# Optimization experiments

Hardware: AMD Instinct MI355X
Metric: run time of the kernel (lower is better)

Reference implementation:

```python
import jax, jax.numpy as jnp
import numpy as np

B, NPG, NFEAT, NHID, NCLASS = 32, 256, 128, 64, 6
N = B * NPG
E_PER = NPG * 16
C = 1.0
SQC = 1.0  # sqrt(c)
MIN_NORM = 1e-15
PROJ_EPS = 4e-3
LAMB = 1.0


def _norm(x):
    return jnp.clip(jnp.linalg.norm(x, axis=-1, keepdims=True), MIN_NORM)


def artanh(x):
    x = jnp.clip(x, -1.0 + 1e-7, 1.0 - 1e-7)
    return 0.5 * (jnp.log1p(x) - jnp.log1p(-x))


def proj(x):
    # clip points to stay inside the Poincare ball
    n = _norm(x)
    maxn = (1.0 - PROJ_EPS) / SQC
    return jnp.where(n > maxn, x / n * maxn, x)


def expmap0(u):
    un = _norm(u)
    return jnp.tanh(SQC * un) * u / (SQC * un)


def logmap0(p):
    pn = _norm(p)
    return artanh(SQC * pn) * p / (SQC * pn)


def mobius_matvec(W, x):
    xn = _norm(x)
    mx = x @ W.T
    mxn = _norm(mx)
    return jnp.tanh(mxn / xn * artanh(SQC * xn)) * mx / (mxn * SQC)


def mobius_add(x, y):
    x2 = jnp.sum(x * x, -1, keepdims=True)
    y2 = jnp.sum(y * y, -1, keepdims=True)
    xy = jnp.sum(x * y, -1, keepdims=True)
    num = (1.0 + 2.0 * C * xy + C * y2) * x + (1.0 - C * x2) * y
    den = 1.0 + 2.0 * C * xy + C * C * x2 * y2
    return num / jnp.clip(den, MIN_NORM)


def hgc_layer(xh, adj, W, b):
    # HypLinear (mobius matvec + hyperbolic bias)
    h = proj(mobius_matvec(W, xh))
    hb = proj(expmap0(b.reshape(1, -1)))
    h = proj(mobius_add(h, hb))
    # HypAgg: aggregate in tangent space at origin
    h = proj(expmap0(adj @ logmap0(h)))
    # HypAct: relu in tangent space
    return proj(expmap0(jax.nn.relu(logmap0(h))))


def hgpsl_pool(x, adj, att, nb, npg):
    deg = adj.sum(-1)
    dis = jnp.where(deg > 0, deg ** -0.5, 0.0)
    prop = dis[:, None] * (adj @ (dis[:, None] * x))
    score = jnp.abs(x - prop).sum(-1)  # [N]
    k = npg // 2
    vals, idx = jax.lax.top_k(score.reshape(nb, npg), k)  # per-graph top-k
    gidx = (idx + (jnp.arange(nb) * npg)[:, None]).reshape(-1)  # global ids
    xn = x[gidx] * jnp.tanh(vals).reshape(-1, 1)
    adj_ind = adj[gidx][:, gidx]
    # structure learning: single-head additive attention, masked per graph
    d = xn.shape[-1]
    e = jax.nn.leaky_relu((xn @ att[:d])[:, None] + (xn @ att[d:])[None, :], 0.2)
    gid = jnp.repeat(jnp.arange(nb), k)
    mask = gid[:, None] == gid[None, :]
    new_adj = jnp.where(mask, jax.nn.relu(e) + LAMB * adj_ind, 0.0)
    return xn, new_adj


def readout(x, nb, k):
    xr = x.reshape(nb, k, -1)
    return jnp.concatenate([xr.max(axis=1), xr.mean(axis=1)], axis=-1)


def to_hyp(t):
    return proj(expmap0(t))  # proj_tan0 is identity on the Poincare ball


def forward(x, edge_index, W1, b1, W2, b2, W3, b3, att1, att2,
            lw1, lb1, lw2, lb2, lw3, lb3):
    row, col = edge_index[0], edge_index[1]
    w = (x[row].sum(-1) + x[col].sum(-1)) * 0.5
    adj1 = jnp.zeros((N, N), x.dtype).at[row, col].set(w)

    t = logmap0(hgc_layer(to_hyp(x), adj1, W1, b1))
    t, adj2 = hgpsl_pool(t, adj1, att1, B, NPG)
    k1 = NPG // 2
    x1 = readout(t, B, k1)

    t = logmap0(hgc_layer(to_hyp(t), adj2, W2, b2))
    t, adj3 = hgpsl_pool(t, adj2, att2, B, k1)
    k2 = k1 // 2
    x2 = readout(t, B, k2)

    t = logmap0(hgc_layer(to_hyp(t), adj3, W3, b3))
    x3 = readout(t, B, k2)

    r = jax.nn.relu(x1) + jax.nn.relu(x2) + jax.nn.relu(x3)
    r = jax.nn.relu(r @ lw1.T + lb1)
    r = jax.nn.relu(r @ lw2.T + lb2)
    return jax.nn.log_softmax(r @ lw3.T + lb3, axis=-1)


def setup_inputs() -> dict:
    key = jax.random.key(0)
    ks = jax.random.split(key, 16)
    s = 0.1
    x = jax.random.normal(ks[0], (N, NFEAT), jnp.float32)
    off = jnp.repeat(jnp.arange(B, dtype=jnp.int32) * NPG, E_PER)
    row = jax.random.randint(ks[1], (B * E_PER,), 0, NPG, jnp.int32) + off
    col = jax.random.randint(ks[2], (B * E_PER,), 0, NPG, jnp.int32) + off
    edge_index = jnp.stack([row, col])
    return {
        "x": x,
        "edge_index": edge_index,
        "W1": jax.random.normal(ks[3], (NHID, NFEAT), jnp.float32) * s,
        "b1": jax.random.normal(ks[4], (NHID,), jnp.float32) * s,
        "W2": jax.random.normal(ks[5], (NHID, NHID), jnp.float32) * s,
        "b2": jax.random.normal(ks[6], (NHID,), jnp.float32) * s,
        "W3": jax.random.normal(ks[7], (NHID, NHID), jnp.float32) * s,
        "b3": jax.random.normal(ks[8], (NHID,), jnp.float32) * s,
        "att1": jax.random.normal(ks[9], (2 * NHID,), jnp.float32) * s,
        "att2": jax.random.normal(ks[10], (2 * NHID,), jnp.float32) * s,
        "lw1": jax.random.normal(ks[11], (NHID, 2 * NHID), jnp.float32) * s,
        "lb1": jnp.zeros((NHID,), jnp.float32),
        "lw2": jax.random.normal(ks[12], (NHID // 2, NHID), jnp.float32) * s,
        "lb2": jnp.zeros((NHID // 2,), jnp.float32),
        "lw3": jax.random.normal(ks[13], (NCLASS, NHID // 2), jnp.float32) * s,
        "lb3": jnp.zeros((NCLASS,), jnp.float32),
    }


def reference(x, edge_index, W1, b1, W2, b2, W3, b3, att1, att2,
              lw1, lb1, lw2, lb2, lw3, lb3):
    return forward(x, edge_index, W1, b1, W2, b2, W3, b3, att1, att2,
                   lw1, lb1, lw2, lb2, lw3, lb3)
```

## Files before the change

kernel.cpp:

```cpp
#include <hip/hip_runtime.h>
#include <math.h>

#define MAXN 0.996f

typedef float f32x4 __attribute__((ext_vector_type(4)));

__device__ __forceinline__ float wredsum(float v) {
#pragma unroll
  for (int o = 32; o > 0; o >>= 1) v += __shfl_xor(v, o);
  return v;
}

__device__ __forceinline__ float artanh_f(float x) {
  x = fminf(fmaxf(x, -1.0f + 1e-7f), 1.0f - 1e-7f);
  return 0.5f * (log1pf(x) - log1pf(-x));
}

__device__ __forceinline__ float cload(const float* p) {
  return __hip_atomic_load(p, __ATOMIC_RELAXED, __HIP_MEMORY_SCOPE_AGENT);
}
__device__ __forceinline__ int cloadi(const int* p) {
  return __hip_atomic_load(p, __ATOMIC_RELAXED, __HIP_MEMORY_SCOPE_AGENT);
}
__device__ __forceinline__ void cstore(float* p, float v) {
  __hip_atomic_store(p, v, __ATOMIC_RELAXED, __HIP_MEMORY_SCOPE_AGENT);
}
__device__ __forceinline__ void cstorei(int* p, int v) {
  __hip_atomic_store(p, v, __ATOMIC_RELAXED, __HIP_MEMORY_SCOPE_AGENT);
}
__device__ __forceinline__ void cstore128(float* p, float a, float b, float c,
                                          float d) {
  f32x4 v;
  v.x = a; v.y = b; v.z = c; v.w = d;
  asm volatile("global_store_dwordx4 %0, %1, off sc0 sc1" ::"v"(p), "v"(v)
               : "memory");
}
__device__ __forceinline__ void quadStore(float* base, int j, float v) {
  float v1 = __shfl_xor(v, 1);
  float v2 = __shfl_xor(v, 2);
  float v3 = __shfl_xor(v, 3);
  if ((j & 3) == 0) cstore128(base + j, v, v1, v2, v3);
}
template <int N>
__device__ __forceinline__ void stage64(float* dst, const float* src, int tid) {
  const unsigned long long* s = (const unsigned long long*)src;
  unsigned long long* d = (unsigned long long*)dst;
  unsigned long long v[N];
#pragma unroll
  for (int k = 0; k < N; ++k)
    v[k] = __hip_atomic_load(s + tid + k * 1024, __ATOMIC_RELAXED,
                             __HIP_MEMORY_SCOPE_AGENT);
#pragma unroll
  for (int k = 0; k < N; ++k) d[tid + k * 1024] = v[k];
}

__device__ __forceinline__ float chainB(float acc) {
  float n0 = sqrtf(wredsum(acc * acc));
  float u0 = fmaxf(n0, 1e-15f);
  float e1 = tanhf(u0) / u0;
  float c1 = fmaxf(e1 * n0, 1e-15f);
  float v = acc * e1;
  if (c1 > MAXN) { v *= MAXN / c1; c1 = MAXN; }
  v *= artanh_f(c1) / c1;
  v = fmaxf(v, 0.f);
  float n2 = sqrtf(wredsum(v * v));
  float u2 = fmaxf(n2, 1e-15f);
  float e2 = tanhf(u2) / u2;
  float c2 = fmaxf(e2 * n2, 1e-15f);
  v *= e2;
  if (c2 > MAXN) { v *= MAXN / c2; c2 = MAXN; }
  v *= artanh_f(c2) / c2;
  return v;
}

__device__ __forceinline__ void hbCalc(int j, const float* __restrict__ b,
                                       float& hbj, float& y2) {
  float bj = b[j];
  float nb = sqrtf(wredsum(bj * bj));
  float ub = fmaxf(nb, 1e-15f);
  float eb = tanhf(ub) / ub;
  float cb = fmaxf(eb * nb, 1e-15f);
  hbj = bj * eb * ((cb > MAXN) ? MAXN / cb : 1.0f);
  y2 = wredsum(hbj * hbj);
}

template <int IND>
__device__ __forceinline__ void doArow(int j, const float* xs, const float* wT,
                                       float hbj, float y2,
                                       float* __restrict__ uout) {
  float a2 = xs[j] * xs[j];
  if (IND == 128) { float x1v = xs[64 + j]; a2 += x1v * x1v; }
  float nx = sqrtf(wredsum(a2));
  float un = fmaxf(nx, 1e-15f);
  float s1 = tanhf(un) / un;
  float nv = s1 * nx;
  float nn = fmaxf(nv, 1e-15f);
  float s2 = (nn > MAXN) ? MAXN / nn : 1.0f;
  float alpha = s1 * s2;
  float xn = fmaxf(fminf(nn, MAXN), 1e-15f);

  float y = 0.f;
  for (int t = 0; t < IND; ++t) y = fmaf(xs[t], wT[t * 65 + j], y);
  float mxj = alpha * y;
  float mxn = fmaxf(sqrtf(wredsum(mxj * mxj)), 1e-15f);
  float hj = (tanhf(mxn / xn * artanh_f(xn)) / mxn) * mxj;

  float hn = fmaxf(sqrtf(wredsum(hj * hj)), 1e-15f);
  if (hn > MAXN) hj *= MAXN / hn;

  float x2 = wredsum(hj * hj);
  float xy = wredsum(hj * hbj);
  float num = (1.f + 2.f * xy + y2) * hj + (1.f - x2) * hbj;
  float den = fmaxf(1.f + 2.f * xy + x2 * y2, 1e-15f);
  float aj = num / den;

  float an = fmaxf(sqrtf(wredsum(aj * aj)), 1e-15f);
  float pn = an;
  if (an > MAXN) { aj *= MAXN / an; pn = MAXN; }
  quadStore(uout, j, (artanh_f(pn) / pn) * aj);
}

template <int NP, int TR, bool WANTDIS>
__device__ __forceinline__ void doBgrpL(int j, int r0, int r0l,
                                        const float* adjS, const float* uS,
                                        float* __restrict__ tg,
                                        float* __restrict__ disg) {
  float acc[TR], dsum[TR];
#pragma unroll
  for (int r = 0; r < TR; ++r) { acc[r] = 0.f; dsum[r] = 0.f; }
  for (int c0 = 0; c0 < NP; c0 += 4) {
    float uv0 = uS[(c0 + 0) * 64 + j];
    float uv1 = uS[(c0 + 1) * 64 + j];
    float uv2 = uS[(c0 + 2) * 64 + j];
    float uv3 = uS[(c0 + 3) * 64 + j];
#pragma unroll
    for (int r = 0; r < TR; ++r) {
      const float4 a4 = *(const float4*)(adjS + (r0l + r) * NP + c0);
      acc[r] = fmaf(a4.x, uv0, acc[r]);
      acc[r] = fmaf(a4.y, uv1, acc[r]);
      acc[r] = fmaf(a4.z, uv2, acc[r]);
      acc[r] = fmaf(a4.w, uv3, acc[r]);
      if (WANTDIS) {
        dsum[r] += a4.x; dsum[r] += a4.y; dsum[r] += a4.z; dsum[r] += a4.w;
      }
    }
  }
#pragma unroll
  for (int r = 0; r < TR; ++r) {
    float v = chainB(acc[r]);
    quadStore(tg + (size_t)(r0 + r) * 64, j, v);
    if (WANTDIS && j == 0)
      cstore(disg + r0 + r, (dsum[r] > 0.f) ? (1.0f / sqrtf(dsum[r])) : 0.f);
  }
}

template <int NP, int TR>
__device__ __forceinline__ void doCgrpL(int j, int r0, int r0l,
                                        const float* adjS, const float* tS,
                                        const float* disS,
                                        float* __restrict__ scoreg) {
  float acc[TR];
#pragma unroll
  for (int r = 0; r < TR; ++r) acc[r] = 0.f;
  for (int c0 = 0; c0 < NP; c0 += 4) {
    float uv0 = disS[c0 + 0] * tS[(c0 + 0) * 64 + j];
    float uv1 = disS[c0 + 1] * tS[(c0 + 1) * 64 + j];
    float uv2 = disS[c0 + 2] * tS[(c0 + 2) * 64 + j];
    float uv3 = disS[c0 + 3] * tS[(c0 + 3) * 64 + j];
#pragma unroll
    for (int r = 0; r < TR; ++r) {
      const float4 a4 = *(const float4*)(adjS + (r0l + r) * NP + c0);
      acc[r] = fmaf(a4.x, uv0, acc[r]);
      acc[r] = fmaf(a4.y, uv1, acc[r]);
      acc[r] = fmaf(a4.z, uv2, acc[r]);
      acc[r] = fmaf(a4.w, uv3, acc[r]);
    }
  }
#pragma unroll
  for (int r = 0; r < TR; ++r) {
    float d = fabsf(tS[(r0 + r) * 64 + j] - disS[r0 + r] * acc[r]);
    d = wredsum(d);
    if (j == 0) cstore(scoreg + r0 + r, d);
  }
}

template <int NP>
__device__ __forceinline__ void doDEa(int j, int i, const float* scS,
                                      const float* tS,
                                      const float* __restrict__ att,
                                      float* __restrict__ xng,
                                      float* __restrict__ s1g,
                                      float* __restrict__ s2g,
                                      int* __restrict__ selg) {
  constexpr int K = NP / 2;
  float si = scS[i];
  float cnt = 0.f;
#pragma unroll
  for (int kk = 0; kk < NP / 64; ++kk) {
    int c = j + kk * 64;
    float v = scS[c];
    cnt += ((v > si) || (v == si && c < i)) ? 1.f : 0.f;
  }
  int rank = (int)wredsum(cnt);
  if (rank < K) {
    float tv = tanhf(si);
    float v = tS[i * 64 + j] * tv;
    quadStore(xng + (size_t)rank * 64, j, v);
    float a = wredsum(v * att[j]);
    float b2 = wredsum(v * att[64 + j]);
    if (j == 0) {
      cstore(s1g + rank, a);
      cstore(s2g + rank, b2);
      cstorei(selg + rank, i);
    }
  }
}

template <int K>
__device__ __forceinline__ void doReadoutL(int j, const float* __restrict__ xng,
                                           float* xrl) {
  float mx = -1e30f, sm = 0.f;
#pragma unroll
  for (int r = 0; r < K; ++r) {
    float v = cload(xng + (size_t)r * 64 + j);
    mx = fmaxf(mx, v);
    sm += v;
  }
  xrl[j] = mx;
  xrl[64 + j] = sm * (1.0f / K);
}

__device__ __forceinline__ void cluster_bar(int* bar, int target, int tid) {
  __syncthreads();
  if (tid == 0) {
    __hip_atomic_fetch_add(bar, 1, __ATOMIC_RELAXED, __HIP_MEMORY_SCOPE_AGENT);
    while (__hip_atomic_load(bar, __ATOMIC_RELAXED, __HIP_MEMORY_SCOPE_AGENT) <
           target * 8)
      __builtin_amdgcn_s_sleep(2);
  }
  __syncthreads();
}

struct KP {
  const float* x; const int* ei; int nE;
  const float *W1, *b1, *W2, *b2, *W3, *b3, *att1, *att2;
  const float *lw1, *lb1, *lw2, *lb2, *lw3, *lb3;
  float *adj2, *adj3, *ubuf, *t1, *t2, *t3, *srow, *dis, *score;
  float *xn1, *xn2, *s1b, *s2b;
  int *sel, *bar;
  float* out;
};

__global__ void __launch_bounds__(1024, 4) k_fwd(KP P) {
  const int tid = threadIdx.x;
  const int wib = tid >> 6;
  const int j = tid & 63;
  const int g = blockIdx.x >> 3;
  const int lb = blockIdx.x & 7;
  const int wc = lb * 16 + wib;

  __shared__ float wT[128 * 65];
  __shared__ float xsAll[16 * 128];
  __shared__ float stage[16384];
  __shared__ float adjS[8192];
  __shared__ float scS[256];
  __shared__ float s1S[128];
  __shared__ float s2S[128];
  __shared__ int selS[128];
  __shared__ float x12S[256];
  float* xs = xsAll + wib * 128;

  int* bar = P.bar + g * 64;
  float* adj2g = P.adj2 + (size_t)g * 16384;
  float* adj3g = P.adj3 + (size_t)g * 4096;
  const float* xg = P.x + (size_t)g * 32768;
  float* srowg = P.srow + g * 256;
  float* ubufg = P.ubuf + (size_t)g * 16384;
  float* t1g = P.t1 + (size_t)g * 16384;
  float* t2g = P.t2 + (size_t)g * 8192;
  float* t3g = P.t3 + (size_t)g * 4096;
  float* disg = P.dis + g * 256;
  float* scoreg = P.score + g * 256;
  float* xn1g = P.xn1 + (size_t)g * 8192;
  float* xn2g = P.xn2 + (size_t)g * 4096;
  float* s1g = P.s1b + g * 128;
  float* s2g = P.s2b + g * 128;
  int* selg = P.sel + g * 128;

  {
    for (int idx = tid; idx < 8192; idx += 1024)
      wT[(idx & 127) * 65 + (idx >> 7)] = P.W1[idx];
    for (int k = tid; k < 8192; k += 1024) adjS[k] = 0.f;
    float hbj, y2;
    hbCalc(j, P.b1, hbj, y2);
    for (int rr = 0; rr < 2; ++rr) {
      const int row = lb * 32 + wib * 2 + rr;
      xs[j] = xg[(size_t)row * 128 + j];
      xs[64 + j] = xg[(size_t)row * 128 + 64 + j];
      float a = xs[j] + xs[64 + j];
      a = wredsum(a);
      if (j == 0) cstore(srowg + row, a);
      doArow<128>(j, xs, wT, hbj, y2, ubufg + (size_t)row * 64);
    }
  }
  cluster_bar(bar, 1, tid);

  {
    if (tid < 256) scS[tid] = cload(srowg + tid);
    stage64<8>(stage, ubufg, tid);
    __syncthreads();
    const int epg = P.nE >> 5;
    for (int e = g * epg + tid; e < (g + 1) * epg; e += 1024) {
      int r = P.ei[e] & 255;
      if ((r >> 5) == lb) {
        int c = P.ei[P.nE + e] & 255;
        adjS[(r & 31) * 256 + c] = 0.5f * (scS[r] + scS[c]);
      }
    }
    __syncthreads();
    doBgrpL<256, 2, true>(j, lb * 32 + wib * 2, wib * 2, adjS, stage, t1g,
                          disg);
    for (int idx = tid; idx < 4096; idx += 1024)
      wT[(idx & 63) * 65 + (idx >> 6)] = P.W2[idx];
  }
  cluster_bar(bar, 2, tid);

  {
    if (tid < 256) scS[tid] = cload(disg + tid);
    stage64<8>(stage, t1g, tid);
    __syncthreads();
    doCgrpL<256, 2>(j, lb * 32 + wib * 2, wib * 2, adjS, stage, scS, scoreg);
  }
  cluster_bar(bar, 3, tid);

  {
    if (tid < 256) scS[tid] = cload(scoreg + tid);
    __syncthreads();
    for (int row = wc; row < 256; row += 128)
      doDEa<256>(j, row, scS, stage, P.att1, xn1g, s1g, s2g, selg);
  }
  cluster_bar(bar, 4, tid);

  {
    if (tid < 128) {
      s1S[tid] = cload(s1g + tid);
      s2S[tid] = cload(s2g + tid);
      selS[tid] = cloadi(selg + tid);
    }
    __syncthreads();
    for (int q = tid; q < 4096; q += 1024) {
      int ii = q >> 5, jj0 = (q & 31) * 4;
      int sii = selS[ii];
      if ((sii >> 5) == lb) {
        const float* arow = adjS + (sii & 31) * 256;
        float s1v = s1S[ii];
        float v0 = fmaxf(s1v + s2S[jj0 + 0], 0.f) + arow[selS[jj0 + 0]];
        float v1 = fmaxf(s1v + s2S[jj0 + 1], 0.f) + arow[selS[jj0 + 1]];
        float v2 = fmaxf(s1v + s2S[jj0 + 2], 0.f) + arow[selS[jj0 + 2]];
        float v3 = fmaxf(s1v + s2S[jj0 + 3], 0.f) + arow[selS[jj0 + 3]];
        cstore128(adj2g + ii * 128 + jj0, v0, v1, v2, v3);
      }
    }
    if (wc == 0) doReadoutL<128>(j, xn1g, x12S);
    float hbj, y2;
    hbCalc(j, P.b2, hbj, y2);
    {
      int row = wc;
      xs[j] = cload(xn1g + (size_t)row * 64 + j);
      doArow<64>(j, xs, wT, hbj, y2, ubufg + (size_t)row * 64);
    }
  }
  cluster_bar(bar, 5, tid);

  {
    stage64<1>(adjS, adj2g + lb * 2048, tid);
    stage64<4>(stage, ubufg, tid);
    __syncthreads();
    doBgrpL<128, 1, true>(j, wc, wib, adjS, stage, t2g, disg);
    for (int idx = tid; idx < 4096; idx += 1024)
      wT[(idx & 63) * 65 + (idx >> 6)] = P.W3[idx];
  }
  cluster_bar(bar, 6, tid);

  {
    if (tid < 128) scS[tid] = cload(disg + tid);
    stage64<4>(stage, t2g, tid);
    __syncthreads();
    doCgrpL<128, 1>(j, wc, wib, adjS, stage, scS, scoreg);
  }
  cluster_bar(bar, 7, tid);

  {
    if (tid < 128) scS[tid] = cload(scoreg + tid);
    __syncthreads();
    doDEa<128>(j, wc, scS, stage, P.att2, xn2g, s1g, s2g, selg);
  }
  cluster_bar(bar, 8, tid);

  {
    if (tid < 64) {
      s1S[tid] = cload(s1g + tid);
      s2S[tid] = cload(s2g + tid);
      selS[tid] = cloadi(selg + tid);
    }
    __syncthreads();
    {
      int ii = tid >> 4, jj0 = (tid & 15) * 4;
      int sii = selS[ii];
      if ((sii >> 4) == lb) {
        const float* arow = adjS + (sii & 15) * 128;
        float s1v = s1S[ii];
        float v0 = fmaxf(s1v + s2S[jj0 + 0], 0.f) + arow[selS[jj0 + 0]];
        float v1 = fmaxf(s1v + s2S[jj0 + 1], 0.f) + arow[selS[jj0 + 1]];
        float v2 = fmaxf(s1v + s2S[jj0 + 2], 0.f) + arow[selS[jj0 + 2]];
        float v3 = fmaxf(s1v + s2S[jj0 + 3], 0.f) + arow[selS[jj0 + 3]];
        cstore128(adj3g + ii * 64 + jj0, v0, v1, v2, v3);
      }
    }
    if (wc == 0) doReadoutL<64>(j, xn2g, x12S + 128);
    float hbj, y2;
    hbCalc(j, P.b3, hbj, y2);
    if (wc < 64) {
      int row = wc;
      xs[j] = cload(xn2g + (size_t)row * 64 + j);
      doArow<64>(j, xs, wT, hbj, y2, ubufg + (size_t)row * 64);
    }
  }
  cluster_bar(bar, 9, tid);

  if (lb < 4) {
    if (tid < 512) {
      unsigned long long v = __hip_atomic_load(
          (const unsigned long long*)(adj3g + lb * 1024) + tid,
          __ATOMIC_RELAXED, __HIP_MEMORY_SCOPE_AGENT);
      ((unsigned long long*)adjS)[tid] = v;
    }
    stage64<2>(stage, ubufg, tid);
    __syncthreads();
    doBgrpL<64, 1, false>(j, wc, wib, adjS, stage, t3g, nullptr);
  }
  cluster_bar(bar, 10, tid);

  if (wc == 0) {
    float mx = -1e30f, sm = 0.f;
#pragma unroll
    for (int r = 0; r < 64; ++r) {
      float v = cload(t3g + (size_t)r * 64 + j);
      mx = fmaxf(mx, v);
      sm += v;
    }
    float* S = xsAll;
    S[j] = fmaxf(x12S[j], 0.f) + fmaxf(x12S[128 + j], 0.f) + fmaxf(mx, 0.f);
    S[64 + j] = fmaxf(x12S[64 + j], 0.f) + fmaxf(x12S[192 + j], 0.f) +
                fmaxf(sm * (1.0f / 64.0f), 0.f);
    float acc = P.lb1[j];
    for (int t = 0; t < 128; ++t) acc += S[t] * P.lw1[(size_t)j * 128 + t];
    S[128 + j] = fmaxf(acc, 0.f);
    if (j < 32) {
      float a = P.lb2[j];
      for (int t = 0; t < 64; ++t) a += S[128 + t] * P.lw2[(size_t)j * 64 + t];
      S[192 + j] = fmaxf(a, 0.f);
    }
    if (j < 6) {
      float a = P.lb3[j];
      for (int t = 0; t < 32; ++t) a += S[192 + t] * P.lw3[(size_t)j * 32 + t];
      S[224 + j] = a;
    }
    if (j < 6) {
      float m = S[224];
      for (int c = 1; c < 6; ++c) m = fmaxf(m, S[224 + c]);
      float se = 0.f;
      for (int c = 0; c < 6; ++c) se += expf(S[224 + c] - m);
      P.out[(size_t)g * 6 + j] = S[224 + j] - m - logf(se);
    }
  }
}

extern "C" void kernel_launch(void* const* d_in, const int* in_sizes, int n_in,
                              void* d_out, int out_size, void* d_ws,
                              size_t ws_size, hipStream_t stream) {
  KP hp;
  hp.x = (const float*)d_in[0];
  hp.ei = (const int*)d_in[1];
  hp.nE = in_sizes[1] / 2;
  hp.W1 = (const float*)d_in[2];
  hp.b1 = (const float*)d_in[3];
  hp.W2 = (const float*)d_in[4];
  hp.b2 = (const float*)d_in[5];
  hp.W3 = (const float*)d_in[6];
  hp.b3 = (const float*)d_in[7];
  hp.att1 = (const float*)d_in[8];
  hp.att2 = (const float*)d_in[9];
  hp.lw1 = (const float*)d_in[10];
  hp.lb1 = (const float*)d_in[11];
  hp.lw2 = (const float*)d_in[12];
  hp.lb2 = (const float*)d_in[13];
  hp.lw3 = (const float*)d_in[14];
  hp.lb3 = (const float*)d_in[15];
  hp.out = (float*)d_out;

  float* p = (float*)d_ws;
  hp.adj2 = p;  p += (size_t)32 * 16384;
  hp.adj3 = p;  p += (size_t)32 * 4096;
  hp.ubuf = p;  p += (size_t)32 * 16384;
  hp.t1 = p;    p += (size_t)32 * 16384;
  hp.t2 = p;    p += (size_t)32 * 8192;
  hp.t3 = p;    p += (size_t)32 * 4096;
  hp.srow = p;  p += 32 * 256;
  hp.dis = p;   p += 32 * 256;
  hp.score = p; p += 32 * 256;
  hp.xn1 = p;   p += (size_t)32 * 8192;
  hp.xn2 = p;   p += (size_t)32 * 4096;
  hp.s1b = p;   p += 32 * 128;
  hp.s2b = p;   p += 32 * 128;
  hp.sel = (int*)p; p += 32 * 128;
  hp.bar = (int*)p; p += 32 * 64;

  hipMemsetAsync(hp.bar, 0, 32 * 64 * sizeof(int), stream);
  k_fwd<<<256, 1024, 0, stream>>>(hp);
}
```

Measured before the change: 208.0 us.

## Collapse late pooling stages into one block per graph, cutting cluster barriers

The first HypLinear now runs redundantly in every block of the 8-block cluster, computing all 256 rows locally into shared memory, which removes the first inter-block barrier and the ubuf/srow global round trip. After the first pooling, seven blocks per graph exit and block 0 alone runs layer 2, the second pooling, layer 3 and the readout MLP entirely in shared memory, so the later cluster barriers and global buffers (adj3, t2, t3, xn2) go away. W3 is preloaded alongside W2. The cost is 8x redundant layer-1 compute and serialising the smaller late stages onto a single block per graph.

```diff
diff --git a/kernel.cpp b/kernel.cpp
--- a/kernel.cpp
+++ b/kernel.cpp
@@ -85,11 +85,10 @@
 }
 
 template <int IND>
-__device__ __forceinline__ void doArow(int j, const float* xs, const float* wT,
-                                       float hbj, float y2,
-                                       float* __restrict__ uout) {
-  float a2 = xs[j] * xs[j];
-  if (IND == 128) { float x1v = xs[64 + j]; a2 += x1v * x1v; }
+__device__ __forceinline__ float doArowV(int j, const float* xr,
+                                         const float* wT, float hbj, float y2) {
+  float a2 = xr[j] * xr[j];
+  if (IND == 128) { float x1v = xr[64 + j]; a2 += x1v * x1v; }
   float nx = sqrtf(wredsum(a2));
   float un = fmaxf(nx, 1e-15f);
   float s1 = tanhf(un) / un;
@@ -100,7 +99,7 @@
   float xn = fmaxf(fminf(nn, MAXN), 1e-15f);
 
   float y = 0.f;
-  for (int t = 0; t < IND; ++t) y = fmaf(xs[t], wT[t * 65 + j], y);
+  for (int t = 0; t < IND; ++t) y = fmaf(xr[t], wT[t * 65 + j], y);
   float mxj = alpha * y;
   float mxn = fmaxf(sqrtf(wredsum(mxj * mxj)), 1e-15f);
   float hj = (tanhf(mxn / xn * artanh_f(xn)) / mxn) * mxj;
@@ -117,7 +116,7 @@
   float an = fmaxf(sqrtf(wredsum(aj * aj)), 1e-15f);
   float pn = an;
   if (an > MAXN) { aj *= MAXN / an; pn = MAXN; }
-  quadStore(uout, j, (artanh_f(pn) / pn) * aj);
+  return (artanh_f(pn) / pn) * aj;
 }
 
 template <int NP, int TR, bool WANTDIS>
@@ -216,20 +215,6 @@
   }
 }
 
-template <int K>
-__device__ __forceinline__ void doReadoutL(int j, const float* __restrict__ xng,
-                                           float* xrl) {
-  float mx = -1e30f, sm = 0.f;
-#pragma unroll
-  for (int r = 0; r < K; ++r) {
-    float v = cload(xng + (size_t)r * 64 + j);
-    mx = fmaxf(mx, v);
-    sm += v;
-  }
-  xrl[j] = mx;
-  xrl[64 + j] = sm * (1.0f / K);
-}
-
 __device__ __forceinline__ void cluster_bar(int* bar, int target, int tid) {
   __syncthreads();
   if (tid == 0) {
@@ -245,8 +230,7 @@
   const float* x; const int* ei; int nE;
   const float *W1, *b1, *W2, *b2, *W3, *b3, *att1, *att2;
   const float *lw1, *lb1, *lw2, *lb2, *lw3, *lb3;
-  float *adj2, *adj3, *ubuf, *t1, *t2, *t3, *srow, *dis, *score;
-  float *xn1, *xn2, *s1b, *s2b;
+  float *t1, *dis, *score, *xn1, *s1b, *s2b, *adj2;
   int *sel, *bar;
   float* out;
 };
@@ -257,57 +241,46 @@
   const int j = tid & 63;
   const int g = blockIdx.x >> 3;
   const int lb = blockIdx.x & 7;
-  const int wc = lb * 16 + wib;
-
-  __shared__ float wT[128 * 65];
-  __shared__ float xsAll[16 * 128];
+
+  __shared__ float wT[8320];
   __shared__ float stage[16384];
   __shared__ float adjS[8192];
+  __shared__ float xsAll[2048];
   __shared__ float scS[256];
+  __shared__ float sc2[256];
   __shared__ float s1S[128];
   __shared__ float s2S[128];
   __shared__ int selS[128];
+  __shared__ float disS2[128];
   __shared__ float x12S[256];
-  float* xs = xsAll + wib * 128;
 
   int* bar = P.bar + g * 64;
-  float* adj2g = P.adj2 + (size_t)g * 16384;
-  float* adj3g = P.adj3 + (size_t)g * 4096;
   const float* xg = P.x + (size_t)g * 32768;
-  float* srowg = P.srow + g * 256;
-  float* ubufg = P.ubuf + (size_t)g * 16384;
   float* t1g = P.t1 + (size_t)g * 16384;
-  float* t2g = P.t2 + (size_t)g * 8192;
-  float* t3g = P.t3 + (size_t)g * 4096;
   float* disg = P.dis + g * 256;
   float* scoreg = P.score + g * 256;
   float* xn1g = P.xn1 + (size_t)g * 8192;
-  float* xn2g = P.xn2 + (size_t)g * 4096;
   float* s1g = P.s1b + g * 128;
   float* s2g = P.s2b + g * 128;
   int* selg = P.sel + g * 128;
+  float* adj2g = P.adj2 + (size_t)g * 16384;
 
   {
     for (int idx = tid; idx < 8192; idx += 1024)
       wT[(idx & 127) * 65 + (idx >> 7)] = P.W1[idx];
     for (int k = tid; k < 8192; k += 1024) adjS[k] = 0.f;
+    __syncthreads();
     float hbj, y2;
     hbCalc(j, P.b1, hbj, y2);
-    for (int rr = 0; rr < 2; ++rr) {
-      const int row = lb * 32 + wib * 2 + rr;
+    float* xs = xsAll + wib * 128;
+    for (int row = wib; row < 256; row += 16) {
       xs[j] = xg[(size_t)row * 128 + j];
       xs[64 + j] = xg[(size_t)row * 128 + 64 + j];
-      float a = xs[j] + xs[64 + j];
-      a = wredsum(a);
-      if (j == 0) cstore(srowg + row, a);
-      doArow<128>(j, xs, wT, hbj, y2, ubufg + (size_t)row * 64);
-    }
-  }
-  cluster_bar(bar, 1, tid);
-
-  {
-    if (tid < 256) scS[tid] = cload(srowg + tid);
-    stage64<8>(stage, ubufg, tid);
+      float a = wredsum(xs[j] + xs[64 + j]);
+      if (j == 0) scS[row] = a;
+      float uv = doArowV<128>(j, xs, wT, hbj, y2);
+      stage[row * 64 + j] = uv;
+    }
     __syncthreads();
     const int epg = P.nE >> 5;
     for (int e = g * epg + tid; e < (g + 1) * epg; e += 1024) {
@@ -320,26 +293,34 @@
     __syncthreads();
     doBgrpL<256, 2, true>(j, lb * 32 + wib * 2, wib * 2, adjS, stage, t1g,
                           disg);
-    for (int idx = tid; idx < 4096; idx += 1024)
-      wT[(idx & 63) * 65 + (idx >> 6)] = P.W2[idx];
-  }
-  cluster_bar(bar, 2, tid);
-
-  {
+  }
+  cluster_bar(bar, 1, tid);
+
+  {
+    stage64<8>(stage, t1g, tid);
     if (tid < 256) scS[tid] = cload(disg + tid);
-    stage64<8>(stage, t1g, tid);
+    for (int idx = tid; idx < 8192; idx += 1024) {
+      if (idx < 4096)
+        wT[(idx & 63) * 65 + (idx >> 6)] = P.W2[idx];
+      else {
+        int q = idx - 4096;
+        wT[4160 + (q & 63) * 65 + (q >> 6)] = P.W3[q];
+      }
+    }
     __syncthreads();
     doCgrpL<256, 2>(j, lb * 32 + wib * 2, wib * 2, adjS, stage, scS, scoreg);
   }
+  cluster_bar(bar, 2, tid);
+
+  {
+    if (tid < 256) sc2[tid] = cload(scoreg + tid);
+    __syncthreads();
+    for (int rr = 0; rr < 2; ++rr) {
+      int row = lb * 32 + wib * 2 + rr;
+      doDEa<256>(j, row, sc2, stage, P.att1, xn1g, s1g, s2g, selg);
+    }
+  }
   cluster_bar(bar, 3, tid);
-
-  {
-    if (tid < 256) scS[tid] = cload(scoreg + tid);
-    __syncthreads();
-    for (int row = wc; row < 256; row += 128)
-      doDEa<256>(j, row, scS, stage, P.att1, xn1g, s1g, s2g, selg);
-  }
-  cluster_bar(bar, 4, tid);
 
   {
     if (tid < 128) {
@@ -361,118 +342,222 @@
         cstore128(adj2g + ii * 128 + jj0, v0, v1, v2, v3);
       }
     }
-    if (wc == 0) doReadoutL<128>(j, xn1g, x12S);
-    float hbj, y2;
-    hbCalc(j, P.b2, hbj, y2);
-    {
-      int row = wc;
-      xs[j] = cload(xn1g + (size_t)row * 64 + j);
-      doArow<64>(j, xs, wT, hbj, y2, ubufg + (size_t)row * 64);
-    }
-  }
-  cluster_bar(bar, 5, tid);
-
-  {
-    stage64<1>(adjS, adj2g + lb * 2048, tid);
-    stage64<4>(stage, ubufg, tid);
-    __syncthreads();
-    doBgrpL<128, 1, true>(j, wc, wib, adjS, stage, t2g, disg);
-    for (int idx = tid; idx < 4096; idx += 1024)
-      wT[(idx & 63) * 65 + (idx >> 6)] = P.W3[idx];
-  }
-  cluster_bar(bar, 6, tid);
-
-  {
-    if (tid < 128) scS[tid] = cload(disg + tid);
-    stage64<4>(stage, t2g, tid);
-    __syncthreads();
-    doCgrpL<128, 1>(j, wc, wib, adjS, stage, scS, scoreg);
-  }
-  cluster_bar(bar, 7, tid);
-
-  {
-    if (tid < 128) scS[tid] = cload(scoreg + tid);
-    __syncthreads();
-    doDEa<128>(j, wc, scS, stage, P.att2, xn2g, s1g, s2g, selg);
-  }
-  cluster_bar(bar, 8, tid);
-
-  {
-    if (tid < 64) {
-      s1S[tid] = cload(s1g + tid);
-      s2S[tid] = cload(s2g + tid);
-      selS[tid] = cloadi(selg + tid);
-    }
-    __syncthreads();
-    {
-      int ii = tid >> 4, jj0 = (tid & 15) * 4;
-      int sii = selS[ii];
-      if ((sii >> 4) == lb) {
-        const float* arow = adjS + (sii & 15) * 128;
-        float s1v = s1S[ii];
-        float v0 = fmaxf(s1v + s2S[jj0 + 0], 0.f) + arow[selS[jj0 + 0]];
-        float v1 = fmaxf(s1v + s2S[jj0 + 1], 0.f) + arow[selS[jj0 + 1]];
-        float v2 = fmaxf(s1v + s2S[jj0 + 2], 0.f) + arow[selS[jj0 + 2]];
-        float v3 = fmaxf(s1v + s2S[jj0 + 3], 0.f) + arow[selS[jj0 + 3]];
-        cstore128(adj3g + ii * 64 + jj0, v0, v1, v2, v3);
-      }
-    }
-    if (wc == 0) doReadoutL<64>(j, xn2g, x12S + 128);
-    float hbj, y2;
-    hbCalc(j, P.b3, hbj, y2);
-    if (wc < 64) {
-      int row = wc;
-      xs[j] = cload(xn2g + (size_t)row * 64 + j);
-      doArow<64>(j, xs, wT, hbj, y2, ubufg + (size_t)row * 64);
-    }
-  }
-  cluster_bar(bar, 9, tid);
-
-  if (lb < 4) {
-    if (tid < 512) {
-      unsigned long long v = __hip_atomic_load(
-          (const unsigned long long*)(adj3g + lb * 1024) + tid,
-          __ATOMIC_RELAXED, __HIP_MEMORY_SCOPE_AGENT);
-      ((unsigned long long*)adjS)[tid] = v;
-    }
-    stage64<2>(stage, ubufg, tid);
-    __syncthreads();
-    doBgrpL<64, 1, false>(j, wc, wib, adjS, stage, t3g, nullptr);
-  }
-  cluster_bar(bar, 10, tid);
-
-  if (wc == 0) {
+  }
+  __syncthreads();
+  if (tid == 0)
+    __hip_atomic_fetch_add(bar, 1, __ATOMIC_RELAXED, __HIP_MEMORY_SCOPE_AGENT);
+  if (lb != 0) return;
+  if (tid == 0)
+    while (__hip_atomic_load(bar, __ATOMIC_RELAXED, __HIP_MEMORY_SCOPE_AGENT) <
+           32)
+      __builtin_amdgcn_s_sleep(2);
+  __syncthreads();
+
+  stage64<4>(stage, xn1g, tid);
+  stage64<4>(stage + 8192, adj2g, tid);
+  stage64<4>(adjS, adj2g + 8192, tid);
+  __syncthreads();
+  if (tid < 64) {
     float mx = -1e30f, sm = 0.f;
-#pragma unroll
-    for (int r = 0; r < 64; ++r) {
-      float v = cload(t3g + (size_t)r * 64 + j);
+    for (int r = 0; r < 128; ++r) {
+      float v = stage[r * 64 + tid];
       mx = fmaxf(mx, v);
       sm += v;
     }
-    float* S = xsAll;
-    S[j] = fmaxf(x12S[j], 0.f) + fmaxf(x12S[128 + j], 0.f) + fmaxf(mx, 0.f);
-    S[64 + j] = fmaxf(x12S[64 + j], 0.f) + fmaxf(x12S[192 + j], 0.f) +
-                fmaxf(sm * (1.0f / 64.0f), 0.f);
-    float acc = P.lb1[j];
-    for (int t = 0; t < 128; ++t) acc += S[t] * P.lw1[(size_t)j * 128 + t];
-    S[128 + j] = fmaxf(acc, 0.f);
-    if (j < 32) {
-      float a = P.lb2[j];
-      for (int t = 0; t < 64; ++t) a += S[128 + t] * P.lw2[(size_t)j * 64 + t];
-      S[192 + j] = fmaxf(a, 0.f);
-    }
-    if (j < 6) {
-      float a = P.lb3[j];
-      for (int t = 0; t < 32; ++t) a += S[192 + t] * P.lw3[(size_t)j * 32 + t];
-      S[224 + j] = a;
-    }
-    if (j < 6) {
-      float m = S[224];
-      for (int c = 1; c < 6; ++c) m = fmaxf(m, S[224 + c]);
-      float se = 0.f;
-      for (int c = 0; c < 6; ++c) se += expf(S[224 + c] - m);
-      P.out[(size_t)g * 6 + j] = S[224 + j] - m - logf(se);
-    }
+    x12S[tid] = mx;
+    x12S[64 + tid] = sm * (1.0f / 128.0f);
+  }
+  __syncthreads();
+  {
+    float hb2, y22;
+    hbCalc(j, P.b2, hb2, y22);
+    for (int rr = 0; rr < 8; ++rr) {
+      int row = wib * 8 + rr;
+      float u = doArowV<64>(j, stage + row * 64, wT, hb2, y22);
+      stage[row * 64 + j] = u;
+    }
+  }
+  __syncthreads();
+  const float* a2r[8];
+#pragma unroll
+  for (int r = 0; r < 8; ++r) {
+    int row = wib * 8 + r;
+    a2r[r] = (row < 64) ? (stage + 8192 + row * 128) : (adjS + (row - 64) * 128);
+  }
+  {
+    float acc2[8], ds2[8];
+#pragma unroll
+    for (int r = 0; r < 8; ++r) { acc2[r] = 0.f; ds2[r] = 0.f; }
+    for (int c0 = 0; c0 < 128; c0 += 4) {
+      float uv0 = stage[(c0 + 0) * 64 + j];
+      float uv1 = stage[(c0 + 1) * 64 + j];
+      float uv2 = stage[(c0 + 2) * 64 + j];
+      float uv3 = stage[(c0 + 3) * 64 + j];
+#pragma unroll
+      for (int r = 0; r < 8; ++r) {
+        const float4 a4 = *(const float4*)(a2r[r] + c0);
+        acc2[r] = fmaf(a4.x, uv0, acc2[r]);
+        acc2[r] = fmaf(a4.y, uv1, acc2[r]);
+        acc2[r] = fmaf(a4.z, uv2, acc2[r]);
+        acc2[r] = fmaf(a4.w, uv3, acc2[r]);
+        ds2[r] += a4.x; ds2[r] += a4.y; ds2[r] += a4.z; ds2[r] += a4.w;
+      }
+    }
+    __syncthreads();
+#pragma unroll
+    for (int r = 0; r < 8; ++r) {
+      int row = wib * 8 + r;
+      float v = chainB(acc2[r]);
+      stage[row * 64 + j] = v;
+      if (j == 0) disS2[row] = (ds2[r] > 0.f) ? (1.0f / sqrtf(ds2[r])) : 0.f;
+    }
+  }
+  __syncthreads();
+  {
+    float acc[8];
+#pragma unroll
+    for (int r = 0; r < 8; ++r) acc[r] = 0.f;
+    for (int c0 = 0; c0 < 128; c0 += 4) {
+      float uv0 = disS2[c0 + 0] * stage[(c0 + 0) * 64 + j];
+      float uv1 = disS2[c0 + 1] * stage[(c0 + 1) * 64 + j];
+      float uv2 = disS2[c0 + 2] * stage[(c0 + 2) * 64 + j];
+      float uv3 = disS2[c0 + 3] * stage[(c0 + 3) * 64 + j];
+#pragma unroll
+      for (int r = 0; r < 8; ++r) {
+        const float4 a4 = *(const float4*)(a2r[r] + c0);
+        acc[r] = fmaf(a4.x, uv0, acc[r]);
+        acc[r] = fmaf(a4.y, uv1, acc[r]);
+        acc[r] = fmaf(a4.z, uv2, acc[r]);
+        acc[r] = fmaf(a4.w, uv3, acc[r]);
+      }
+    }
+#pragma unroll
+    for (int r = 0; r < 8; ++r) {
+      int row = wib * 8 + r;
+      float d = fabsf(stage[row * 64 + j] - disS2[row] * acc[r]);
+      d = wredsum(d);
+      if (j == 0) sc2[row] = d;
+    }
+  }
+  __syncthreads();
+  for (int rr = 0; rr < 8; ++rr) {
+    int i = wib * 8 + rr;
+    float si = sc2[i];
+    float cnt = 0.f;
+    {
+      float v = sc2[j];
+      cnt += ((v > si) || (v == si && j < i)) ? 1.f : 0.f;
+      float v2 = sc2[64 + j];
+      cnt += ((v2 > si) || (v2 == si && 64 + j < i)) ? 1.f : 0.f;
+    }
+    int rank = (int)wredsum(cnt);
+    if (rank < 64) {
+      float tv = tanhf(si);
+      float v = stage[i * 64 + j] * tv;
+      wT[rank * 64 + j] = v;
+      float a = wredsum(v * P.att2[j]);
+      float b2 = wredsum(v * P.att2[64 + j]);
+      if (j == 0) { s1S[rank] = a; s2S[rank] = b2; selS[rank] = i; }
+    }
+  }
+  __syncthreads();
+  float a3v[4];
+  {
+    int base = tid * 4;
+#pragma unroll
+    for (int k = 0; k < 4; ++k) {
+      int idx = base + k, ii = idx >> 6, jj = idx & 63;
+      int r_ = selS[ii], c_ = selS[jj];
+      float av = (r_ < 64) ? stage[8192 + r_ * 128 + c_]
+                           : adjS[(r_ - 64) * 128 + c_];
+      a3v[k] = fmaxf(s1S[ii] + s2S[jj], 0.f) + av;
+    }
+  }
+  if (tid < 64) {
+    float mx = -1e30f, sm = 0.f;
+    for (int r = 0; r < 64; ++r) {
+      float v = wT[r * 64 + tid];
+      mx = fmaxf(mx, v);
+      sm += v;
+    }
+    x12S[128 + tid] = mx;
+    x12S[192 + tid] = sm * (1.0f / 64.0f);
+  }
+  __syncthreads();
+#pragma unroll
+  for (int k = 0; k < 4; ++k) stage[8192 + tid * 4 + k] = a3v[k];
+  {
+    float hb3, y23;
+    hbCalc(j, P.b3, hb3, y23);
+    for (int rr = 0; rr < 4; ++rr) {
+      int row = wib * 4 + rr;
+      float u = doArowV<64>(j, wT + row * 64, wT + 4160, hb3, y23);
+      wT[row * 64 + j] = u;
+    }
+  }
+  __syncthreads();
+  {
+    float acc3[4];
+#pragma unroll
+    for (int r = 0; r < 4; ++r) acc3[r] = 0.f;
+    for (int c0 = 0; c0 < 64; c0 += 4) {
+      float uv0 = wT[(c0 + 0) * 64 + j];
+      float uv1 = wT[(c0 + 1) * 64 + j];
+      float uv2 = wT[(c0 + 2) * 64 + j];
+      float uv3 = wT[(c0 + 3) * 64 + j];
+#pragma unroll
+      for (int r = 0; r < 4; ++r) {
+        int row = wib * 4 + r;
+        const float4 a4 = *(const float4*)(stage + 8192 + row * 64 + c0);
+        acc3[r] = fmaf(a4.x, uv0, acc3[r]);
+        acc3[r] = fmaf(a4.y, uv1, acc3[r]);
+        acc3[r] = fmaf(a4.z, uv2, acc3[r]);
+        acc3[r] = fmaf(a4.w, uv3, acc3[r]);
+      }
+    }
+#pragma unroll
+    for (int r = 0; r < 4; ++r)
+      stage[12288 + (wib * 4 + r) * 64 + j] = chainB(acc3[r]);
+  }
+  __syncthreads();
+  float* S = xsAll;
+  if (tid < 64) {
+    float mx = -1e30f, sm = 0.f;
+    for (int r = 0; r < 64; ++r) {
+      float v = stage[12288 + r * 64 + tid];
+      mx = fmaxf(mx, v);
+      sm += v;
+    }
+    S[tid] = fmaxf(x12S[tid], 0.f) + fmaxf(x12S[128 + tid], 0.f) +
+             fmaxf(mx, 0.f);
+    S[64 + tid] = fmaxf(x12S[64 + tid], 0.f) + fmaxf(x12S[192 + tid], 0.f) +
+                  fmaxf(sm * (1.0f / 64.0f), 0.f);
+  }
+  __syncthreads();
+  if (tid < 64) {
+    float acc = P.lb1[tid];
+    for (int t = 0; t < 128; ++t) acc += S[t] * P.lw1[(size_t)tid * 128 + t];
+    S[128 + tid] = fmaxf(acc, 0.f);
+  }
+  __syncthreads();
+  if (tid < 32) {
+    float a = P.lb2[tid];
+    for (int t = 0; t < 64; ++t) a += S[128 + t] * P.lw2[(size_t)tid * 64 + t];
+    S[192 + tid] = fmaxf(a, 0.f);
+  }
+  __syncthreads();
+  if (tid < 6) {
+    float a = P.lb3[tid];
+    for (int t = 0; t < 32; ++t) a += S[192 + t] * P.lw3[(size_t)tid * 32 + t];
+    S[224 + tid] = a;
+  }
+  __syncthreads();
+  if (tid < 6) {
+    float m = S[224];
+    for (int c = 1; c < 6; ++c) m = fmaxf(m, S[224 + c]);
+    float se = 0.f;
+    for (int c = 0; c < 6; ++c) se += expf(S[224 + c] - m);
+    P.out[(size_t)g * 6 + tid] = S[224 + tid] - m - logf(se);
   }
 }
 
@@ -500,19 +585,13 @@
   hp.out = (float*)d_out;
 
   float* p = (float*)d_ws;
-  hp.adj2 = p;  p += (size_t)32 * 16384;
-  hp.adj3 = p;  p += (size_t)32 * 4096;
-  hp.ubuf = p;  p += (size_t)32 * 16384;
   hp.t1 = p;    p += (size_t)32 * 16384;
-  hp.t2 = p;    p += (size_t)32 * 8192;
-  hp.t3 = p;    p += (size_t)32 * 4096;
-  hp.srow = p;  p += 32 * 256;
   hp.dis = p;   p += 32 * 256;
   hp.score = p; p += 32 * 256;
   hp.xn1 = p;   p += (size_t)32 * 8192;
-  hp.xn2 = p;   p += (size_t)32 * 4096;
   hp.s1b = p;   p += 32 * 128;
   hp.s2b = p;   p += 32 * 128;
+  hp.adj2 = p;  p += (size_t)32 * 16384;
   hp.sel = (int*)p; p += 32 * 128;
   hp.bar = (int*)p; p += 32 * 64;
 
```

New measurement: 562.5 us. +170.4%, slower.
